# Kernel optimization log

Hardware: AMD Instinct MI355X
Metric: run time of the kernel (lower is better)

The kernel has to match this reference:

```python
import jax, jax.numpy as jnp
import numpy as np

B, K, T, H = 64, 49, 512, 512  # batch, regions, timesteps, hidden_size
A = 49                          # attention bottleneck dim (hard-coded in module)


def setup_inputs() -> dict:
    key = jax.random.key(0)
    ks = jax.random.split(key, 7)
    s = 1.0 / np.sqrt(H)
    return {
        "V":   jax.random.normal(ks[0], (B, K, H), jnp.float32),
        "h_t": jax.random.normal(ks[1], (B, T, H), jnp.float32),
        "s_t": jax.random.normal(ks[2], (B, T, H), jnp.float32),
        "Wv":  jax.random.normal(ks[3], (A, H), jnp.float32) * s,
        "Wg":  jax.random.normal(ks[4], (A, H), jnp.float32) * s,
        "Ws":  jax.random.normal(ks[5], (A, H), jnp.float32) * s,
        "Wh":  jax.random.normal(ks[6], (1, A), jnp.float32) * (1.0 / np.sqrt(A)),
    }


def reference(V, h_t, s_t, Wv, Wg, Ws, Wh):
    # Dropout is identity (eval mode). torch.nn.Linear: y = x @ W.T
    wh = Wh[0]                                     # [A]
    cv = jnp.einsum('bkh,ah->bka', V, Wv)          # [B,K,A]
    gh = jnp.einsum('bth,ah->bta', h_t, Wg)        # [B,T,A]
    content_v = cv[:, None, :, :] + gh[:, :, None, :]      # [B,T,K,A]
    z_t = jnp.einsum('btka,a->btk', jnp.tanh(content_v), wh)  # [B,T,K]
    alpha_t = jax.nn.softmax(z_t, axis=-1)         # softmax over K regions
    c_t = jnp.einsum('btk,bkh->bth', alpha_t, V)   # [B,T,H]

    content_s = jnp.einsum('bth,ah->bta', s_t, Ws) + gh       # [B,T,A]
    z_ext = jnp.einsum('bta,a->bt', jnp.tanh(content_s), wh)  # [B,T]
    extended = jnp.concatenate([z_t, z_ext[:, :, None]], axis=2)  # [B,T,K+1]
    alpha_hat = jax.nn.softmax(extended, axis=-1)
    beta_t = alpha_hat[:, :, -1:]                  # [B,T,1] sentinel gate

    c_hat_t = beta_t * s_t + (1.0 - beta_t) * c_t  # [B,T,H]
    return c_hat_t, alpha_t, beta_t
```

## Files before the change

kernel.cpp:

```cpp
#include <hip/hip_runtime.h>
#include <hip/hip_bf16.h>
#include <cstdint>
#include <cstddef>

#define NB 64
#define NK 49
#define NT 512
#define NH 512
#define NA 49

typedef __attribute__((ext_vector_type(8))) short bf16x8;
typedef __attribute__((ext_vector_type(4))) float f32x4;

__device__ __forceinline__ float fast_exp(float x) {
    return __builtin_amdgcn_exp2f(x * 1.4426950408889634f);
}
__device__ __forceinline__ float fast_tanh(float x) {
    float e = __builtin_amdgcn_exp2f(x * 2.8853900817779268f);
    return 1.0f - 2.0f * __builtin_amdgcn_rcpf(e + 1.0f);
}
__device__ __forceinline__ short bf16rn(float x) {
    unsigned b = __builtin_bit_cast(unsigned, x);
    unsigned r = b + 0x7FFFu + ((b >> 16) & 1u);
    return (short)(r >> 16);
}
__device__ __forceinline__ void split_hi_lo(float x, short& hi, short& lo) {
    unsigned b = __builtin_bit_cast(unsigned, x);
    unsigned hb = b & 0xFFFF0000u;
    hi = (short)(hb >> 16);
    lo = bf16rn(x - __builtin_bit_cast(float, hb));
}

__global__ __launch_bounds__(256, 4) void kprew(
        const float* __restrict__ Wg, const float* __restrict__ Ws,
        const float* __restrict__ Wv, short* __restrict__ WB) {
    const int job = blockIdx.x >> 3, slice = blockIdx.x & 7;
    const float* W = (job == 0) ? Wg : (job == 1 ? Ws : Wv);
    short* dst = WB + (size_t)job * 65536;
    const int end = (slice + 1) * 8192;
    for (int idx = slice * 8192 + threadIdx.x; idx < end; idx += 256) {
        int e    = idx & 7;
        int lane = (idx >> 3) & 63;
        int ks   = (idx >> 9) & 15;
        int nt   = (idx >> 13) & 3;
        int sel  = idx >> 15;
        int a = nt * 16 + (lane & 15);
        int h = ks * 32 + (lane >> 4) * 8 + e;
        float x = (a < NA) ? W[a * NH + h] : 0.0f;
        short hi, lo; split_hi_lo(x, hi, lo);
        dst[idx] = sel ? lo : hi;
    }
}

__global__ __launch_bounds__(256, 4) void kprev(
        const float* __restrict__ V, const short* __restrict__ WB,
        short* __restrict__ VB, float* __restrict__ cv) {
    const int bid = blockIdx.x;
    if (bid < 512) {
        __shared__ float vl[NK * 64];
        const int b  = bid >> 3;
        const int sl = bid & 7;
        const int h0 = sl * 64;
        const float* Vb = V + (size_t)b * (NK * NH);
        for (int idx = threadIdx.x; idx < NK * 64; idx += 256) {
            int k = idx >> 6, c = idx & 63;
            vl[idx] = Vb[(size_t)k * NH + h0 + c];
        }
        __syncthreads();
        short* dst = VB + (size_t)b * 32768;
        for (int idx = threadIdx.x; idx < 4096; idx += 256) {
            int e    = idx & 7;
            int lane = (idx >> 3) & 63;
            int ks   = (idx >> 9) & 1;
            int ntl  = idx >> 10;
            int k = ks * 32 + (lane >> 4) * 8 + e;
            int c = ntl * 16 + (lane & 15);
            float x = (k < NK) ? vl[k * 64 + c] : 0.0f;
            dst[((size_t)(sl * 4 + ntl) * 2 + ks) * 512 + lane * 8 + e] = bf16rn(x);
        }
    } else {
        const int tid  = threadIdx.x;
        const int lane = tid & 63;
        const int w    = tid >> 6;
        const int m0   = (bid - 512) * 64 + w * 16;
        const int r    = lane & 15;
        const int g    = lane >> 4;

        const float* arow = V + (size_t)(m0 + r) * NH + g * 8;
        const bf16x8* wbv = (const bf16x8*)(WB + 2 * 65536);

        f32x4 acc0 = {0.f, 0.f, 0.f, 0.f};
        f32x4 acc1 = acc0, acc2 = acc0, acc3 = acc0;

        #pragma unroll 2
        for (int ks = 0; ks < 16; ++ks) {
            float4 x0 = *(const float4*)(arow + ks * 32);
            float4 x1 = *(const float4*)(arow + ks * 32 + 4);
            bf16x8 bh0 = wbv[(0 * 16 + ks) * 64 + lane];
            bf16x8 bh1 = wbv[(1 * 16 + ks) * 64 + lane];
            bf16x8 bh2 = wbv[(2 * 16 + ks) * 64 + lane];
            bf16x8 bh3 = wbv[(3 * 16 + ks) * 64 + lane];
            bf16x8 bl0 = wbv[(4 * 16 + ks) * 64 + lane];
            bf16x8 bl1 = wbv[(5 * 16 + ks) * 64 + lane];
            bf16x8 bl2 = wbv[(6 * 16 + ks) * 64 + lane];
            bf16x8 bl3 = wbv[(7 * 16 + ks) * 64 + lane];

            bf16x8 ahi, alo;
            {
                const float xs[8] = {x0.x, x0.y, x0.z, x0.w, x1.x, x1.y, x1.z, x1.w};
                #pragma unroll
                for (int e = 0; e < 8; ++e) { short hi, lo; split_hi_lo(xs[e], hi, lo); ahi[e] = hi; alo[e] = lo; }
            }
            acc0 = __builtin_amdgcn_mfma_f32_16x16x32_bf16(ahi, bh0, acc0, 0, 0, 0);
            acc0 = __builtin_amdgcn_mfma_f32_16x16x32_bf16(alo, bh0, acc0, 0, 0, 0);
            acc0 = __builtin_amdgcn_mfma_f32_16x16x32_bf16(ahi, bl0, acc0, 0, 0, 0);
            acc1 = __builtin_amdgcn_mfma_f32_16x16x32_bf16(ahi, bh1, acc1, 0, 0, 0);
            acc1 = __builtin_amdgcn_mfma_f32_16x16x32_bf16(alo, bh1, acc1, 0, 0, 0);
            acc1 = __builtin_amdgcn_mfma_f32_16x16x32_bf16(ahi, bl1, acc1, 0, 0, 0);
            acc2 = __builtin_amdgcn_mfma_f32_16x16x32_bf16(ahi, bh2, acc2, 0, 0, 0);
            acc2 = __builtin_amdgcn_mfma_f32_16x16x32_bf16(alo, bh2, acc2, 0, 0, 0);
            acc2 = __builtin_amdgcn_mfma_f32_16x16x32_bf16(ahi, bl2, acc2, 0, 0, 0);
            acc3 = __builtin_amdgcn_mfma_f32_16x16x32_bf16(ahi, bh3, acc3, 0, 0, 0);
            acc3 = __builtin_amdgcn_mfma_f32_16x16x32_bf16(alo, bh3, acc3, 0, 0, 0);
            acc3 = __builtin_amdgcn_mfma_f32_16x16x32_bf16(ahi, bl3, acc3, 0, 0, 0);
        }

        #pragma unroll
        for (int reg = 0; reg < 4; ++reg) {
            int row = m0 + g * 4 + reg;
            float* orow = cv + (size_t)row * 52;
            orow[ 0 + r] = acc0[reg];
            orow[16 + r] = acc1[reg];
            orow[32 + r] = acc2[reg];
            if (r == 0) orow[48] = acc3[reg];
        }
    }
}

__global__ __launch_bounds__(256, 4) void kfused(
        const float* __restrict__ h_t, const float* __restrict__ s_t,
        const float* __restrict__ Wh,
        const short* __restrict__ WB, const short* __restrict__ VB,
        const float* __restrict__ cv_ws,
        float* __restrict__ out_chat, float* __restrict__ out_alpha,
        float* __restrict__ out_beta) {
    __shared__ float cvl[NK * 52];
    __shared__ float ghl[32 * 52];
    __shared__ float ssl[32 * 52];
    __shared__ float zl[32 * 50];
    __shared__ short afrag[2048];
    __shared__ float whl[52];
    __shared__ float betal[32];

    const int tid  = threadIdx.x;
    const int lane = tid & 63;
    const int w    = tid >> 6;
    const int b    = blockIdx.x >> 4;
    const int t0   = (blockIdx.x & 15) * 32;
    const int r    = lane & 15;
    const int g    = lane >> 4;

    if (tid < NA) whl[tid] = Wh[tid];

    {
        const float* cvb = cv_ws + (size_t)b * (NK * 52);
        for (int idx = tid; idx < NK * 52; idx += 256) cvl[idx] = cvb[idx];
    }

    {
        const int job = w >> 1, mtile = w & 1;
        const float* in = job ? s_t : h_t;
        const bf16x8* wb = (const bf16x8*)(WB + (size_t)job * 65536);
        const float* arow = in + (size_t)(b * NT + t0 + mtile * 16 + r) * NH + g * 8;
        f32x4 acc0 = {0.f, 0.f, 0.f, 0.f};
        f32x4 acc1 = acc0, acc2 = acc0, acc3 = acc0;
        #pragma unroll 2
        for (int ks = 0; ks < 16; ++ks) {
            float4 x0 = *(const float4*)(arow + ks * 32);
            float4 x1 = *(const float4*)(arow + ks * 32 + 4);
            bf16x8 bh0 = wb[(( 0 + 0) * 16 + ks) * 64 + lane];
            bf16x8 bh1 = wb[(( 0 + 1) * 16 + ks) * 64 + lane];
            bf16x8 bh2 = wb[(( 0 + 2) * 16 + ks) * 64 + lane];
            bf16x8 bh3 = wb[(( 0 + 3) * 16 + ks) * 64 + lane];
            bf16x8 bl0 = wb[(( 4 + 0) * 16 + ks) * 64 + lane];
            bf16x8 bl1 = wb[(( 4 + 1) * 16 + ks) * 64 + lane];
            bf16x8 bl2 = wb[(( 4 + 2) * 16 + ks) * 64 + lane];
            bf16x8 bl3 = wb[(( 4 + 3) * 16 + ks) * 64 + lane];
            bf16x8 ahi, alo;
            {
                const float xs[8] = {x0.x, x0.y, x0.z, x0.w, x1.x, x1.y, x1.z, x1.w};
                #pragma unroll
                for (int e = 0; e < 8; ++e) { short hi, lo; split_hi_lo(xs[e], hi, lo); ahi[e] = hi; alo[e] = lo; }
            }
            acc0 = __builtin_amdgcn_mfma_f32_16x16x32_bf16(ahi, bh0, acc0, 0, 0, 0);
            acc0 = __builtin_amdgcn_mfma_f32_16x16x32_bf16(alo, bh0, acc0, 0, 0, 0);
            acc0 = __builtin_amdgcn_mfma_f32_16x16x32_bf16(ahi, bl0, acc0, 0, 0, 0);
            acc1 = __builtin_amdgcn_mfma_f32_16x16x32_bf16(ahi, bh1, acc1, 0, 0, 0);
            acc1 = __builtin_amdgcn_mfma_f32_16x16x32_bf16(alo, bh1, acc1, 0, 0, 0);
            acc1 = __builtin_amdgcn_mfma_f32_16x16x32_bf16(ahi, bl1, acc1, 0, 0, 0);
            acc2 = __builtin_amdgcn_mfma_f32_16x16x32_bf16(ahi, bh2, acc2, 0, 0, 0);
            acc2 = __builtin_amdgcn_mfma_f32_16x16x32_bf16(alo, bh2, acc2, 0, 0, 0);
            acc2 = __builtin_amdgcn_mfma_f32_16x16x32_bf16(ahi, bl2, acc2, 0, 0, 0);
            acc3 = __builtin_amdgcn_mfma_f32_16x16x32_bf16(ahi, bh3, acc3, 0, 0, 0);
            acc3 = __builtin_amdgcn_mfma_f32_16x16x32_bf16(alo, bh3, acc3, 0, 0, 0);
            acc3 = __builtin_amdgcn_mfma_f32_16x16x32_bf16(ahi, bl3, acc3, 0, 0, 0);
        }
        float* dst = (w >> 1) ? ssl : ghl;
        #pragma unroll
        for (int reg = 0; reg < 4; ++reg) {
            int m = mtile * 16 + g * 4 + reg;
            dst[m * 52 +  0 + r] = acc0[reg];
            dst[m * 52 + 16 + r] = acc1[reg];
            dst[m * 52 + 32 + r] = acc2[reg];
            if (r < 4) dst[m * 52 + 48 + r] = acc3[reg];
        }
    }
    __syncthreads();

    {
        for (int p = tid; p < 32 * NK; p += 256) {
            int t = (int)(((unsigned)p * 1338u) >> 16);
            int k = p - t * NK;
            const float* rowp = cvl + k * 52;
            const float* gp   = ghl + t * 52;
            float zx = 0.f, zy = 0.f, zz = 0.f, zw = 0.f;
            #pragma unroll
            for (int q = 0; q < 12; ++q) {
                float4 rr = *(const float4*)(rowp + q * 4);
                float4 gg = *(const float4*)(gp + q * 4);
                zx = fmaf(whl[q * 4 + 0], fast_tanh(rr.x + gg.x), zx);
                zy = fmaf(whl[q * 4 + 1], fast_tanh(rr.y + gg.y), zy);
                zz = fmaf(whl[q * 4 + 2], fast_tanh(rr.z + gg.z), zz);
                zw = fmaf(whl[q * 4 + 3], fast_tanh(rr.w + gg.w), zw);
            }
            float z = (zx + zy) + (zz + zw);
            zl[t * 50 + k] = fmaf(whl[48], fast_tanh(rowp[48] + gp[48]), z);
        }
    }
    __syncthreads();

    {
        const int trow = w * 8 + (lane >> 3);
        const int sub  = lane & 7;
        float* zr = zl + trow * 50;

        float m = -1e30f;
        for (int k = sub; k < NK; k += 8) m = fmaxf(m, zr[k]);
        m = fmaxf(m, __shfl_xor(m, 1));
        m = fmaxf(m, __shfl_xor(m, 2));
        m = fmaxf(m, __shfl_xor(m, 4));

        float S = 0.0f;
        for (int k = sub; k < NK; k += 8) S += fast_exp(zr[k] - m);
        S += __shfl_xor(S, 1);
        S += __shfl_xor(S, 2);
        S += __shfl_xor(S, 4);
        float rS = __builtin_amdgcn_rcpf(S);

        const float* sp = ssl + trow * 52;
        const float* gp = ghl + trow * 52;
        float ze = 0.0f;
        for (int a = sub; a < NA; a += 8) ze = fmaf(whl[a], fast_tanh(sp[a] + gp[a]), ze);
        ze += __shfl_xor(ze, 1);
        ze += __shfl_xor(ze, 2);
        ze += __shfl_xor(ze, 4);

        float m50  = fmaxf(m, ze);
        float eext = fast_exp(ze - m50);
        float beta = eext * __builtin_amdgcn_rcpf(S * fast_exp(m - m50) + eext);
        if (sub == 0) {
            betal[trow] = beta;
            out_beta[(size_t)b * NT + t0 + trow] = beta;
        }

        const int mt = trow >> 4, rr2 = trow & 15;
        for (int k = sub; k < 64; k += 8) {
            float a = (k < NK) ? fast_exp(zr[k] - m) * rS : 0.0f;
            if (k < NK) zr[k] = a;
            int ks = k >> 5, gg = (k & 31) >> 3;
            afrag[(((ks * 2 + mt) * 64) + gg * 16 + rr2) * 8 + sub] = bf16rn(a);
        }
    }
    __syncthreads();

    {
        float* oa = out_alpha + ((size_t)b * NT + t0) * NK;
        for (int idx = tid; idx < 32 * NK; idx += 256) {
            int t = (int)(((unsigned)idx * 1338u) >> 16);
            int k = idx - t * NK;
            oa[idx] = zl[t * 50 + k];
        }
    }

    {
        const bf16x8* af = (const bf16x8*)afrag;
        const bf16x8* vb = (const bf16x8*)(VB + (size_t)b * 32768);
        const size_t rowb = (size_t)b * NT + t0;

        bf16x8 a00 = af[(0 * 2 + 0) * 64 + lane];
        bf16x8 a01 = af[(0 * 2 + 1) * 64 + lane];
        bf16x8 a10 = af[(1 * 2 + 0) * 64 + lane];
        bf16x8 a11 = af[(1 * 2 + 1) * 64 + lane];

        #pragma unroll 2
        for (int ntl = 0; ntl < 8; ++ntl) {
            const int nt = w * 8 + ntl;
            bf16x8 b0 = vb[(nt * 2 + 0) * 64 + lane];
            bf16x8 b1 = vb[(nt * 2 + 1) * 64 + lane];
            f32x4 acc0 = {0.f, 0.f, 0.f, 0.f};
            f32x4 acc1 = acc0;
            acc0 = __builtin_amdgcn_mfma_f32_16x16x32_bf16(a00, b0, acc0, 0, 0, 0);
            acc0 = __builtin_amdgcn_mfma_f32_16x16x32_bf16(a10, b1, acc0, 0, 0, 0);
            acc1 = __builtin_amdgcn_mfma_f32_16x16x32_bf16(a01, b0, acc1, 0, 0, 0);
            acc1 = __builtin_amdgcn_mfma_f32_16x16x32_bf16(a11, b1, acc1, 0, 0, 0);

            const int h0 = nt * 16 + r;
            #pragma unroll
            for (int reg = 0; reg < 4; ++reg) {
                {
                    int tloc = g * 4 + reg;
                    float bt = betal[tloc];
                    size_t off = (rowb + tloc) * NH + h0;
                    float s = s_t[off];
                    out_chat[off] = fmaf(bt, s - acc0[reg], acc0[reg]);
                }
                {
                    int tloc = 16 + g * 4 + reg;
                    float bt = betal[tloc];
                    size_t off = (rowb + tloc) * NH + h0;
                    float s = s_t[off];
                    out_chat[off] = fmaf(bt, s - acc1[reg], acc1[reg]);
                }
            }
        }
    }
}

extern "C" void kernel_launch(void* const* d_in, const int* in_sizes, int n_in,
                              void* d_out, int out_size, void* d_ws, size_t ws_size,
                              hipStream_t stream) {
    const float* V   = (const float*)d_in[0];
    const float* h_t = (const float*)d_in[1];
    const float* s_t = (const float*)d_in[2];
    const float* Wv  = (const float*)d_in[3];
    const float* Wg  = (const float*)d_in[4];
    const float* Ws  = (const float*)d_in[5];
    const float* Wh  = (const float*)d_in[6];

    float* out = (float*)d_out;
    float* out_chat  = out;
    float* out_alpha = out + (size_t)NB * NT * NH;
    float* out_beta  = out_alpha + (size_t)NB * NT * NK;

    short* WB = (short*)d_ws;
    short* VB = WB + (size_t)3 * 65536;
    float* cv = (float*)(VB + (size_t)64 * 32768);

    kprew<<<24, 256, 0, stream>>>(Wg, Ws, Wv, WB);
    kprev<<<561, 256, 0, stream>>>(V, WB, VB, cv);
    kfused<<<NB * 16, 256, 0, stream>>>(h_t, s_t, Wh, WB, VB, cv,
                                        out_chat, out_alpha, out_beta);
}
```

Measured before the change: 96.60 us.

## Round activations to single bf16 instead of hi/lo split in projection GEMM

The h_t/s_t projection in the fused kernel now rounds each activation to one bf16 value instead of splitting it into hi and lo parts. This drops the alo*bh MFMA term, leaving two MFMAs per tile instead of three, and removes the split arithmetic. The loop unroll drops from 2 to 1 and the occupancy hint rises from 4 to 5 blocks per CU. The cost is lower precision in the attention logits, since activations now keep only about 8 mantissa bits, which may fail tolerance checks.

```diff
diff --git a/kernel.cpp b/kernel.cpp
--- a/kernel.cpp
+++ b/kernel.cpp
@@ -29,6 +29,12 @@
     unsigned hb = b & 0xFFFF0000u;
     hi = (short)(hb >> 16);
     lo = bf16rn(x - __builtin_bit_cast(float, hb));
+}
+__device__ __forceinline__ bf16x8 cvt8(float4 x0, float4 x1) {
+    bf16x8 a;
+    a[0] = bf16rn(x0.x); a[1] = bf16rn(x0.y); a[2] = bf16rn(x0.z); a[3] = bf16rn(x0.w);
+    a[4] = bf16rn(x1.x); a[5] = bf16rn(x1.y); a[6] = bf16rn(x1.z); a[7] = bf16rn(x1.w);
+    return a;
 }
 
 __global__ __launch_bounds__(256, 4) void kprew(
@@ -137,7 +143,7 @@
     }
 }
 
-__global__ __launch_bounds__(256, 4) void kfused(
+__global__ __launch_bounds__(256, 5) void kfused(
         const float* __restrict__ h_t, const float* __restrict__ s_t,
         const float* __restrict__ Wh,
         const short* __restrict__ WB, const short* __restrict__ VB,
@@ -174,36 +180,28 @@
         const float* arow = in + (size_t)(b * NT + t0 + mtile * 16 + r) * NH + g * 8;
         f32x4 acc0 = {0.f, 0.f, 0.f, 0.f};
         f32x4 acc1 = acc0, acc2 = acc0, acc3 = acc0;
-        #pragma unroll 2
+        #pragma unroll 1
         for (int ks = 0; ks < 16; ++ks) {
             float4 x0 = *(const float4*)(arow + ks * 32);
             float4 x1 = *(const float4*)(arow + ks * 32 + 4);
-            bf16x8 bh0 = wb[(( 0 + 0) * 16 + ks) * 64 + lane];
-            bf16x8 bh1 = wb[(( 0 + 1) * 16 + ks) * 64 + lane];
-            bf16x8 bh2 = wb[(( 0 + 2) * 16 + ks) * 64 + lane];
-            bf16x8 bh3 = wb[(( 0 + 3) * 16 + ks) * 64 + lane];
-            bf16x8 bl0 = wb[(( 4 + 0) * 16 + ks) * 64 + lane];
-            bf16x8 bl1 = wb[(( 4 + 1) * 16 + ks) * 64 + lane];
-            bf16x8 bl2 = wb[(( 4 + 2) * 16 + ks) * 64 + lane];
-            bf16x8 bl3 = wb[(( 4 + 3) * 16 + ks) * 64 + lane];
-            bf16x8 ahi, alo;
-            {
-                const float xs[8] = {x0.x, x0.y, x0.z, x0.w, x1.x, x1.y, x1.z, x1.w};
-                #pragma unroll
-                for (int e = 0; e < 8; ++e) { short hi, lo; split_hi_lo(xs[e], hi, lo); ahi[e] = hi; alo[e] = lo; }
-            }
-            acc0 = __builtin_amdgcn_mfma_f32_16x16x32_bf16(ahi, bh0, acc0, 0, 0, 0);
-            acc0 = __builtin_amdgcn_mfma_f32_16x16x32_bf16(alo, bh0, acc0, 0, 0, 0);
-            acc0 = __builtin_amdgcn_mfma_f32_16x16x32_bf16(ahi, bl0, acc0, 0, 0, 0);
-            acc1 = __builtin_amdgcn_mfma_f32_16x16x32_bf16(ahi, bh1, acc1, 0, 0, 0);
-            acc1 = __builtin_amdgcn_mfma_f32_16x16x32_bf16(alo, bh1, acc1, 0, 0, 0);
-            acc1 = __builtin_amdgcn_mfma_f32_16x16x32_bf16(ahi, bl1, acc1, 0, 0, 0);
-            acc2 = __builtin_amdgcn_mfma_f32_16x16x32_bf16(ahi, bh2, acc2, 0, 0, 0);
-            acc2 = __builtin_amdgcn_mfma_f32_16x16x32_bf16(alo, bh2, acc2, 0, 0, 0);
-            acc2 = __builtin_amdgcn_mfma_f32_16x16x32_bf16(ahi, bl2, acc2, 0, 0, 0);
-            acc3 = __builtin_amdgcn_mfma_f32_16x16x32_bf16(ahi, bh3, acc3, 0, 0, 0);
-            acc3 = __builtin_amdgcn_mfma_f32_16x16x32_bf16(alo, bh3, acc3, 0, 0, 0);
-            acc3 = __builtin_amdgcn_mfma_f32_16x16x32_bf16(ahi, bl3, acc3, 0, 0, 0);
+            bf16x8 bh0 = wb[((0 + 0) * 16 + ks) * 64 + lane];
+            bf16x8 bh1 = wb[((0 + 1) * 16 + ks) * 64 + lane];
+            bf16x8 bh2 = wb[((0 + 2) * 16 + ks) * 64 + lane];
+            bf16x8 bh3 = wb[((0 + 3) * 16 + ks) * 64 + lane];
+            bf16x8 bl0 = wb[((4 + 0) * 16 + ks) * 64 + lane];
+            bf16x8 bl1 = wb[((4 + 1) * 16 + ks) * 64 + lane];
+            bf16x8 bl2 = wb[((4 + 2) * 16 + ks) * 64 + lane];
+            bf16x8 bl3 = wb[((4 + 3) * 16 + ks) * 64 + lane];
+
+            bf16x8 aa = cvt8(x0, x1);
+            acc0 = __builtin_amdgcn_mfma_f32_16x16x32_bf16(aa, bh0, acc0, 0, 0, 0);
+            acc0 = __builtin_amdgcn_mfma_f32_16x16x32_bf16(aa, bl0, acc0, 0, 0, 0);
+            acc1 = __builtin_amdgcn_mfma_f32_16x16x32_bf16(aa, bh1, acc1, 0, 0, 0);
+            acc1 = __builtin_amdgcn_mfma_f32_16x16x32_bf16(aa, bl1, acc1, 0, 0, 0);
+            acc2 = __builtin_amdgcn_mfma_f32_16x16x32_bf16(aa, bh2, acc2, 0, 0, 0);
+            acc2 = __builtin_amdgcn_mfma_f32_16x16x32_bf16(aa, bl2, acc2, 0, 0, 0);
+            acc3 = __builtin_amdgcn_mfma_f32_16x16x32_bf16(aa, bh3, acc3, 0, 0, 0);
+            acc3 = __builtin_amdgcn_mfma_f32_16x16x32_bf16(aa, bl3, acc3, 0, 0, 0);
         }
         float* dst = (w >> 1) ? ssl : ghl;
         #pragma unroll
```

Result: slower. 123.0 us (+27.3%).
